# Optimization experiments

Measured on AMD Instinct MI355X. Metric: run time of the kernel, lower is better.

## Reference

```python
import jax, jax.numpy as jnp
import jax.lax as lax
import numpy as np
import math

B, T_FRAMES, H, W = 32, 8, 14, 14
C, CA = 768, 384
L = H * W + 1


def setup_inputs() -> dict:
    key = jax.random.key(0)
    ks = jax.random.split(key, 7)
    s = 0.02
    return {
        "x": jax.random.normal(ks[0], (B * T_FRAMES, L, C), dtype=jnp.float32),
        "W1": jax.random.normal(ks[1], (CA, C), dtype=jnp.float32) * s,
        "b1": jnp.zeros((CA,), dtype=jnp.float32),
        "conv_w": jax.random.normal(ks[2], (CA, 1, 3, 3, 3), dtype=jnp.float32) * s,
        "conv_b": jnp.zeros((CA,), dtype=jnp.float32),
        "W2": jax.random.normal(ks[3], (C, CA), dtype=jnp.float32) * s,
        "b2": jnp.zeros((C,), dtype=jnp.float32),
        "T": T_FRAMES,
    }


def reference(x, W1, b1, conv_w, conv_b, W2, b2, T):
    BT, Lx, Cx = x.shape
    Bb = BT // T
    Ca = W1.shape[0]
    Hh = Ww = int(round(math.sqrt(Lx - 1)))
    # fc1 on all tokens except CLS: [BT, L-1, Ca]
    h = jnp.einsum("blc,ac->bla", x[:, 1:, :], W1) + b1
    # -> [B, Ca, T, H, W] for depthwise 3d conv (groups = Ca)
    h = h.reshape(Bb, T, Hh, Ww, Ca).transpose(0, 4, 1, 2, 3)
    h = lax.conv_general_dilated(
        h, conv_w,
        window_strides=(1, 1, 1),
        padding=[(1, 1), (1, 1), (1, 1)],
        dimension_numbers=("NCDHW", "OIDHW", "NCDHW"),
        feature_group_count=Ca,
    ) + conv_b[None, :, None, None, None]
    # back to [BT, L-1, Ca]
    h = h.transpose(0, 2, 3, 4, 1).reshape(BT, Lx - 1, Ca)
    # fc2: [BT, L-1, C]
    h = jnp.einsum("bla,ca->blc", h, W2) + b2
    # residual add onto non-CLS tokens
    return x.at[:, 1:, :].add(h)
```

## Files before the change

kernel.cpp:

```cpp
#include <hip/hip_runtime.h>
#include <hip/hip_bf16.h>
#include <stdint.h>

#define BTOT   256
#define LX     197
#define CDIM   768
#define CADIM  384
#define TFR    8
#define LM1    196
#define MTOT   50176

typedef unsigned short u16;
typedef short          bf16x8 __attribute__((ext_vector_type(8)));
typedef unsigned short u16x4  __attribute__((ext_vector_type(4)));
typedef unsigned short u16x8  __attribute__((ext_vector_type(8)));
typedef float          f32x4  __attribute__((ext_vector_type(4)));

typedef const __attribute__((address_space(1))) void gvoid_t;
typedef __attribute__((address_space(3))) void       svoid_t;

static __device__ __forceinline__ u16 f2bf(float f) {
  union { float f; uint32_t u; } v; v.f = f;
  uint32_t u = v.u;
  return (u16)((u + 0x7FFFu + ((u >> 16) & 1u)) >> 16);
}
static __device__ __forceinline__ float bf2f(u16 h) {
  union { uint32_t u; float f; } v; v.u = ((uint32_t)h) << 16;
  return v.f;
}
static __device__ __forceinline__ u16 f2bf_hw(float f) {
  union { __hip_bfloat16 b; u16 u; } v;
  v.b = __float2bfloat16(f);
  return v.u;
}

__global__ void prep_small(const float4* __restrict__ x4, float4* __restrict__ out4,
                           const float* __restrict__ W1, const float* __restrict__ W2,
                           const float* __restrict__ cw, u16* __restrict__ w1b,
                           u16* __restrict__ w2b, float* __restrict__ cwT) {
  int i = blockIdx.x * blockDim.x + threadIdx.x;
  if (i < CADIM * CDIM) { w1b[i] = f2bf(W1[i]); w2b[i] = f2bf(W2[i]); }
  if (i < CADIM * 27) {
    int a = i / 27; int tap = i - a * 27;
    cwT[tap * CADIM + a] = cw[i];
  }
  if (i < BTOT * 192) {
    int f = i / 192, v = i - f * 192;
    size_t off = (size_t)f * (LX * CDIM / 4) + v;
    out4[off] = x4[off];
  }
}


__global__ __launch_bounds__(768, 2) void fc1_gemm(
    const float* __restrict__ X,
    const u16* __restrict__ Bw,
    const float* __restrict__ bias,
    u16* __restrict__ Hout)
{
  __shared__ __align__(16) u16 As[2 * 128 * 32];
  __shared__ __align__(16) u16 Bs[2 * 384 * 32];
  const int tid  = threadIdx.x;
  const int lane = tid & 63;
  const int wave = tid >> 6;
  const int m0 = blockIdx.x * 128;
  const int lm = lane & 15;
  const int lk = lane >> 4;
  const int wr = wave / 6;
  const int wc = wave - wr * 6;
  const int wm = wr * 64;
  const int wn = wc * 64;
  const bool is_a = (wave < 4);

  const int g = tid >> 3;
  const int q = tid & 7;
  size_t arow[4];
  int awst[4];
  if (is_a) {
#pragma unroll
    for (int s = 0; s < 4; ++s) {
      int row = g + 32 * s;
      int tok = m0 + row;
      int bt = tok / LM1;
      int l  = tok - bt * LM1;
      arow[s] = (size_t)(bt * LX + 1 + l) * CDIM + q * 4;
      int R    = row >> 1;
      int uu   = (row & 1) * 4 + (q >> 1);
      int slot = uu ^ (R & 7);
      awst[s]  = R * 64 + slot * 8 + (q & 1) * 4;
    }
  }

  const int wb  = wave - 4;
  const int u   = (lane & 7) ^ (lane >> 3);
  const int rr  = 2 * (lane >> 3) + (u >> 2);
  const int cko = (u & 3) * 8;
  size_t boff[3];
  int ldst[3];
  if (!is_a) {
#pragma unroll
    for (int s = 0; s < 3; ++s) {
      int row = wb * 48 + s * 16 + rr;
      boff[s] = (size_t)row * CDIM + cko;
      ldst[s] = (wb * 24 + s * 8) * 64;
    }
  }

  const int lmh   = lm >> 1;
  const int slotp = (((lm & 1) << 2) | lk) ^ lmh;
  const int abase = ((wm >> 1) + lmh) * 64 + slotp * 8;
  const int bbase = ((wn >> 1) + lmh) * 64 + slotp * 8;

  f32x4 acc[4][4];
#pragma unroll
  for (int i = 0; i < 4; i++)
#pragma unroll
    for (int j = 0; j < 4; j++) acc[i][j] = (f32x4)0.0f;

  float4 areg[4];

  if (is_a) {
#pragma unroll
    for (int s = 0; s < 4; ++s) areg[s] = *(const float4*)(X + arow[s]);
#pragma unroll
    for (int s = 0; s < 4; ++s) {
      u16x4 o;
      o[0] = f2bf_hw(areg[s].x); o[1] = f2bf_hw(areg[s].y);
      o[2] = f2bf_hw(areg[s].z); o[3] = f2bf_hw(areg[s].w);
      *(u16x4*)&As[awst[s]] = o;
    }
  } else {
#pragma unroll
    for (int s = 0; s < 3; ++s)
      __builtin_amdgcn_global_load_lds((gvoid_t*)(Bw + boff[s]),
          (svoid_t*)(Bs + ldst[s]), 16, 0, 0);
  }
  __syncthreads();

  int cur = 0;
  for (int kt = 0; kt < 23; ++kt) {
    const int k1 = (kt + 1) * 32;
    const int nb = cur ^ 1;
    if (is_a) {
#pragma unroll
      for (int s = 0; s < 4; ++s) areg[s] = *(const float4*)(X + arow[s] + k1);
    } else {
#pragma unroll
      for (int s = 0; s < 3; ++s)
        __builtin_amdgcn_global_load_lds((gvoid_t*)(Bw + boff[s] + k1),
            (svoid_t*)(Bs + nb * 12288 + ldst[s]), 16, 0, 0);
    }
    {
      const u16* Ab = As + cur * 4096;
      const u16* Bb = Bs + cur * 12288;
      bf16x8 af[4], bfr[4];
#pragma unroll
      for (int i = 0; i < 4; i++) af[i] = *(const bf16x8*)&Ab[abase + i * 512];
#pragma unroll
      for (int j = 0; j < 4; j++) bfr[j] = *(const bf16x8*)&Bb[bbase + j * 512];
#pragma unroll
      for (int i = 0; i < 4; i++)
#pragma unroll
        for (int j = 0; j < 4; j++)
          acc[i][j] = __builtin_amdgcn_mfma_f32_16x16x32_bf16(af[i], bfr[j], acc[i][j], 0, 0, 0);
    }
    if (is_a) {
#pragma unroll
      for (int s = 0; s < 4; ++s) {
        u16x4 o;
        o[0] = f2bf_hw(areg[s].x); o[1] = f2bf_hw(areg[s].y);
        o[2] = f2bf_hw(areg[s].z); o[3] = f2bf_hw(areg[s].w);
        *(u16x4*)&As[nb * 4096 + awst[s]] = o;
      }
    }
    __syncthreads();
    cur ^= 1;
  }
  {
    const u16* Ab = As + cur * 4096;
    const u16* Bb = Bs + cur * 12288;
    bf16x8 af[4], bfr[4];
#pragma unroll
    for (int i = 0; i < 4; i++) af[i] = *(const bf16x8*)&Ab[abase + i * 512];
#pragma unroll
    for (int j = 0; j < 4; j++) bfr[j] = *(const bf16x8*)&Bb[bbase + j * 512];
#pragma unroll
    for (int i = 0; i < 4; i++)
#pragma unroll
      for (int j = 0; j < 4; j++)
        acc[i][j] = __builtin_amdgcn_mfma_f32_16x16x32_bf16(af[i], bfr[j], acc[i][j], 0, 0, 0);
  }

#pragma unroll
  for (int i = 0; i < 4; i++) {
    int rbase = m0 + wm + i * 16 + lk * 4;
#pragma unroll
    for (int j = 0; j < 4; j++) {
      int col = wn + j * 16 + lm;
      float bv = bias[col];
#pragma unroll
      for (int r = 0; r < 4; r++)
        Hout[(rbase + r) * CADIM + col] = f2bf(acc[i][j][r] + bv);
    }
  }
}

__global__ __launch_bounds__(256) void dwconv(
    const u16* __restrict__ h1, const float* __restrict__ cwT,
    const float* __restrict__ cb, u16* __restrict__ h2)
{
  __shared__ __align__(16) u16 lin[3 * 196 * 32];
  const int tid = threadIdx.x;
  const int f   = blockIdx.x;
  const int cc  = blockIdx.y;
  const int tv  = f & 7;

  for (int i = tid; i < 3 * 196 * 4; i += 256) {
    int fd  = i / 784;
    int rem = i - fd * 784;
    int pos = rem >> 2;
    int c8  = rem & 3;
    int tt  = tv + fd - 1;
    u16x8 v = (u16x8)0;
    if (tt >= 0 && tt < TFR) {
      const u16* src = h1 + ((size_t)(f + fd - 1) * LM1 + pos) * CADIM
                          + cc * 32 + c8 * 8;
      v = *(const u16x8*)src;
    }
    *(u16x8*)&lin[(fd * 196 + pos) * 32 + c8 * 8] = v;
  }
  __syncthreads();

  const int cg    = tid & 3;
  const int pidx  = tid >> 2;
  const int cbase = cc * 32 + cg * 8;

  float bv[8];
#pragma unroll
  for (int c = 0; c < 8; ++c) bv[c] = cb[cbase + c];

  float acc[4][8];
  int hk[4], wk[4];
#pragma unroll
  for (int k = 0; k < 4; ++k) {
    int p = pidx + 64 * k;
    hk[k] = p / 14;
    wk[k] = p - hk[k] * 14;
#pragma unroll
    for (int c = 0; c < 8; ++c) acc[k][c] = bv[c];
  }

  for (int dt = 0; dt < 3; ++dt) {
#pragma unroll
    for (int j = 0; j < 9; ++j) {
      const int dh = j / 3 - 1, dw = j % 3 - 1;
      float w8[8];
      const float* wp8 = cwT + (dt * 9 + j) * CADIM + cbase;
#pragma unroll
      for (int c = 0; c < 8; ++c) w8[c] = wp8[c];
#pragma unroll
      for (int k = 0; k < 4; ++k) {
        int p = pidx + 64 * k;
        if (p >= 196) continue;
        int hh = hk[k] + dh, ww = wk[k] + dw;
        if (hh < 0 || hh >= 14 || ww < 0 || ww >= 14) continue;
        const u16x8 v = *(const u16x8*)&lin[(dt * 196 + hh * 14 + ww) * 32 + cg * 8];
#pragma unroll
        for (int c = 0; c < 8; ++c)
          acc[k][c] += bf2f((u16)v[c]) * w8[c];
      }
    }
  }

#pragma unroll
  for (int k = 0; k < 4; ++k) {
    int p = pidx + 64 * k;
    if (p < 196) {
      u16x8 o;
#pragma unroll
      for (int c = 0; c < 8; ++c) o[c] = f2bf(acc[k][c]);
      *(u16x8*)(h2 + ((size_t)f * LM1 + p) * CADIM + cbase) = o;
    }
  }
}

__global__ __launch_bounds__(768, 2) void fc2_gemm(
    const u16* __restrict__ A,
    const u16* __restrict__ Bw,
    const float* __restrict__ bias,
    const float* __restrict__ x,
    float* __restrict__ out)
{
  __shared__ __align__(16) u16 As[2 * 128 * 32];
  __shared__ __align__(16) u16 Bs[2 * 384 * 32];
  const int tid  = threadIdx.x;
  const int lane = tid & 63;
  const int wave = tid >> 6;
  const int m0 = blockIdx.x * 128;
  const int n0 = blockIdx.y * 384;
  const int lm = lane & 15;
  const int lk = lane >> 4;
  const int wr = wave / 6;
  const int wc = wave - wr * 6;
  const int wm = wr * 64;
  const int wn = wc * 64;
  const bool is_a = (wave < 4);

  const int u   = (lane & 7) ^ (lane >> 3);
  const int rr  = 2 * (lane >> 3) + (u >> 2);
  const int cko = (u & 3) * 8;

  size_t aoff[2];
  int lasta[2];
  if (is_a) {
#pragma unroll
    for (int s = 0; s < 2; ++s) {
      int row = wave * 32 + s * 16 + rr;
      aoff[s]  = (size_t)(m0 + row) * CADIM + cko;
      lasta[s] = (wave * 16 + s * 8) * 64;
    }
  }
  const int wb = wave - 4;
  size_t boff[3];
  int ldst[3];
  if (!is_a) {
#pragma unroll
    for (int s = 0; s < 3; ++s) {
      int row = wb * 48 + s * 16 + rr;
      boff[s] = (size_t)(n0 + row) * CADIM + cko;
      ldst[s] = (wb * 24 + s * 8) * 64;
    }
  }

  const int lmh   = lm >> 1;
  const int slotp = (((lm & 1) << 2) | lk) ^ lmh;
  const int abase = ((wm >> 1) + lmh) * 64 + slotp * 8;
  const int bbase = ((wn >> 1) + lmh) * 64 + slotp * 8;

  f32x4 acc[4][4];
#pragma unroll
  for (int i = 0; i < 4; i++)
#pragma unroll
    for (int j = 0; j < 4; j++) acc[i][j] = (f32x4)0.0f;

  if (is_a) {
#pragma unroll
    for (int s = 0; s < 2; ++s)
      __builtin_amdgcn_global_load_lds((gvoid_t*)(A + aoff[s]),
          (svoid_t*)(As + lasta[s]), 16, 0, 0);
  } else {
#pragma unroll
    for (int s = 0; s < 3; ++s)
      __builtin_amdgcn_global_load_lds((gvoid_t*)(Bw + boff[s]),
          (svoid_t*)(Bs + ldst[s]), 16, 0, 0);
  }
  __syncthreads();

  int cur = 0;
  for (int kt = 0; kt < 11; ++kt) {
    const int k1 = (kt + 1) * 32;
    const int nb = cur ^ 1;
    if (is_a) {
#pragma unroll
      for (int s = 0; s < 2; ++s)
        __builtin_amdgcn_global_load_lds((gvoid_t*)(A + aoff[s] + k1),
            (svoid_t*)(As + nb * 4096 + lasta[s]), 16, 0, 0);
    } else {
#pragma unroll
      for (int s = 0; s < 3; ++s)
        __builtin_amdgcn_global_load_lds((gvoid_t*)(Bw + boff[s] + k1),
            (svoid_t*)(Bs + nb * 12288 + ldst[s]), 16, 0, 0);
    }
    {
      const u16* Ab = As + cur * 4096;
      const u16* Bb = Bs + cur * 12288;
      bf16x8 af[4], bfr[4];
#pragma unroll
      for (int i = 0; i < 4; i++) af[i] = *(const bf16x8*)&Ab[abase + i * 512];
#pragma unroll
      for (int j = 0; j < 4; j++) bfr[j] = *(const bf16x8*)&Bb[bbase + j * 512];
#pragma unroll
      for (int i = 0; i < 4; i++)
#pragma unroll
        for (int j = 0; j < 4; j++)
          acc[i][j] = __builtin_amdgcn_mfma_f32_16x16x32_bf16(af[i], bfr[j], acc[i][j], 0, 0, 0);
    }
    __syncthreads();
    cur ^= 1;
  }
  {
    const u16* Ab = As + cur * 4096;
    const u16* Bb = Bs + cur * 12288;
    bf16x8 af[4], bfr[4];
#pragma unroll
    for (int i = 0; i < 4; i++) af[i] = *(const bf16x8*)&Ab[abase + i * 512];
#pragma unroll
    for (int j = 0; j < 4; j++) bfr[j] = *(const bf16x8*)&Bb[bbase + j * 512];
#pragma unroll
    for (int i = 0; i < 4; i++)
#pragma unroll
      for (int j = 0; j < 4; j++)
        acc[i][j] = __builtin_amdgcn_mfma_f32_16x16x32_bf16(af[i], bfr[j], acc[i][j], 0, 0, 0);
  }

  float bve[4];
#pragma unroll
  for (int j = 0; j < 4; j++) bve[j] = bias[n0 + wn + j * 16 + lm];
#pragma unroll
  for (int i = 0; i < 4; i++) {
    int rbase = m0 + wm + i * 16 + lk * 4;
    size_t orow[4];
#pragma unroll
    for (int r = 0; r < 4; r++) {
      int tok = rbase + r;
      int bt = tok / LM1;
      int l  = tok - bt * LM1;
      orow[r] = (size_t)(bt * LX + 1 + l) * CDIM + (n0 + wn + lm);
    }
    float xv[4][4];
#pragma unroll
    for (int r = 0; r < 4; r++)
#pragma unroll
      for (int j = 0; j < 4; j++)
        xv[r][j] = x[orow[r] + j * 16];
#pragma unroll
    for (int r = 0; r < 4; r++)
#pragma unroll
      for (int j = 0; j < 4; j++)
        out[orow[r] + j * 16] = xv[r][j] + acc[i][j][r] + bve[j];
  }
}

extern "C" void kernel_launch(void* const* d_in, const int* in_sizes, int n_in,
                              void* d_out, int out_size, void* d_ws, size_t ws_size,
                              hipStream_t stream) {
  const float* x  = (const float*)d_in[0];
  const float* W1 = (const float*)d_in[1];
  const float* b1 = (const float*)d_in[2];
  const float* cw = (const float*)d_in[3];
  const float* cb = (const float*)d_in[4];
  const float* W2 = (const float*)d_in[5];
  const float* b2 = (const float*)d_in[6];
  float* out = (float*)d_out;

  char* ws = (char*)d_ws;
  u16*   w1b = (u16*)(ws + 0);
  u16*   w2b = (u16*)(ws + 589824);
  float* cwT = (float*)(ws + 1179648);
  u16*   h1  = (u16*)(ws + 1245184);
  u16*   h2  = (u16*)(ws + 39780352);

  prep_small<<<1152, 256, 0, stream>>>((const float4*)x, (float4*)out,
                                       W1, W2, cw, w1b, w2b, cwT);
  fc1_gemm<<<MTOT / 128, 768, 0, stream>>>(x, w1b, b1, h1);
  dwconv  <<<dim3(BTOT, 12), 256, 0, stream>>>(h1, cwT, cb, h2);
  fc2_gemm<<<dim3(MTOT / 128, 2), 768, 0, stream>>>(h2, w2b, b2, x, out);
}
```

Measured before the change: 452.3 us.

## Shrink fc2 GEMM tiles to 128x128 with XCD-aware block swizzle

Result: faster. 434.2 us (-4.0%).

```diff
diff --git a/kernel.cpp b/kernel.cpp
--- a/kernel.cpp
+++ b/kernel.cpp
@@ -284,7 +284,7 @@
   }
 }
 
-__global__ __launch_bounds__(768, 2) void fc2_gemm(
+__global__ __launch_bounds__(256) void fc2_gemm(
     const u16* __restrict__ A,
     const u16* __restrict__ Bw,
     const float* __restrict__ bias,
@@ -292,44 +292,34 @@
     float* __restrict__ out)
 {
   __shared__ __align__(16) u16 As[2 * 128 * 32];
-  __shared__ __align__(16) u16 Bs[2 * 384 * 32];
+  __shared__ __align__(16) u16 Bs[2 * 128 * 32];
   const int tid  = threadIdx.x;
   const int lane = tid & 63;
   const int wave = tid >> 6;
-  const int m0 = blockIdx.x * 128;
-  const int n0 = blockIdx.y * 384;
+
+  const int orig = blockIdx.x;
+  const int lgc  = (orig & 7) * 294 + (orig >> 3);
+  const int lmt  = lgc / 6;
+  const int lnt  = lgc - lmt * 6;
+  const int m0 = lmt * 128;
+  const int n0 = lnt * 128;
+
   const int lm = lane & 15;
   const int lk = lane >> 4;
-  const int wr = wave / 6;
-  const int wc = wave - wr * 6;
-  const int wm = wr * 64;
-  const int wn = wc * 64;
-  const bool is_a = (wave < 4);
+  const int wm = (wave & 1) * 64;
+  const int wn = (wave >> 1) * 64;
 
   const int u   = (lane & 7) ^ (lane >> 3);
   const int rr  = 2 * (lane >> 3) + (u >> 2);
   const int cko = (u & 3) * 8;
-
-  size_t aoff[2];
-  int lasta[2];
-  if (is_a) {
-#pragma unroll
-    for (int s = 0; s < 2; ++s) {
-      int row = wave * 32 + s * 16 + rr;
-      aoff[s]  = (size_t)(m0 + row) * CADIM + cko;
-      lasta[s] = (wave * 16 + s * 8) * 64;
-    }
-  }
-  const int wb = wave - 4;
-  size_t boff[3];
-  int ldst[3];
-  if (!is_a) {
-#pragma unroll
-    for (int s = 0; s < 3; ++s) {
-      int row = wb * 48 + s * 16 + rr;
-      boff[s] = (size_t)(n0 + row) * CADIM + cko;
-      ldst[s] = (wb * 24 + s * 8) * 64;
-    }
+  size_t aoff[2], boff[2];
+  int ldst[2];
+#pragma unroll
+  for (int s = 0; s < 2; ++s) {
+    int row = wave * 32 + s * 16 + rr;
+    aoff[s] = (size_t)(m0 + row) * CADIM + cko;
+    boff[s] = (size_t)(n0 + row) * CADIM + cko;
+    ldst[s] = (wave * 16 + s * 8) * 64;
   }
 
   const int lmh   = lm >> 1;
@@ -343,37 +333,28 @@
 #pragma unroll
     for (int j = 0; j < 4; j++) acc[i][j] = (f32x4)0.0f;
 
-  if (is_a) {
-#pragma unroll
-    for (int s = 0; s < 2; ++s)
-      __builtin_amdgcn_global_load_lds((gvoid_t*)(A + aoff[s]),
-          (svoid_t*)(As + lasta[s]), 16, 0, 0);
-  } else {
-#pragma unroll
-    for (int s = 0; s < 3; ++s)
-      __builtin_amdgcn_global_load_lds((gvoid_t*)(Bw + boff[s]),
-          (svoid_t*)(Bs + ldst[s]), 16, 0, 0);
+#pragma unroll
+  for (int s = 0; s < 2; ++s) {
+    __builtin_amdgcn_global_load_lds((gvoid_t*)(A + aoff[s]),
+        (svoid_t*)(As + ldst[s]), 16, 0, 0);
+    __builtin_amdgcn_global_load_lds((gvoid_t*)(Bw + boff[s]),
+        (svoid_t*)(Bs + ldst[s]), 16, 0, 0);
   }
   __syncthreads();
-
   int cur = 0;
   for (int kt = 0; kt < 11; ++kt) {
     const int k1 = (kt + 1) * 32;
     const int nb = cur ^ 1;
-    if (is_a) {
-#pragma unroll
-      for (int s = 0; s < 2; ++s)
-        __builtin_amdgcn_global_load_lds((gvoid_t*)(A + aoff[s] + k1),
-            (svoid_t*)(As + nb * 4096 + lasta[s]), 16, 0, 0);
-    } else {
-#pragma unroll
-      for (int s = 0; s < 3; ++s)
-        __builtin_amdgcn_global_load_lds((gvoid_t*)(Bw + boff[s] + k1),
-            (svoid_t*)(Bs + nb * 12288 + ldst[s]), 16, 0, 0);
+#pragma unroll
+    for (int s = 0; s < 2; ++s) {
+      __builtin_amdgcn_global_load_lds((gvoid_t*)(A + aoff[s] + k1),
+          (svoid_t*)(As + nb * 4096 + ldst[s]), 16, 0, 0);
+      __builtin_amdgcn_global_load_lds((gvoid_t*)(Bw + boff[s] + k1),
+          (svoid_t*)(Bs + nb * 4096 + ldst[s]), 16, 0, 0);
     }
     {
       const u16* Ab = As + cur * 4096;
-      const u16* Bb = Bs + cur * 12288;
+      const u16* Bb = Bs + cur * 4096;
       bf16x8 af[4], bfr[4];
 #pragma unroll
       for (int i = 0; i < 4; i++) af[i] = *(const bf16x8*)&Ab[abase + i * 512];
@@ -390,7 +371,7 @@
   }
   {
     const u16* Ab = As + cur * 4096;
-    const u16* Bb = Bs + cur * 12288;
+    const u16* Bb = Bs + cur * 4096;
     bf16x8 af[4], bfr[4];
 #pragma unroll
     for (int i = 0; i < 4; i++) af[i] = *(const bf16x8*)&Ab[abase + i * 512];
@@ -403,9 +384,9 @@
         acc[i][j] = __builtin_amdgcn_mfma_f32_16x16x32_bf16(af[i], bfr[j], acc[i][j], 0, 0, 0);
   }
 
-  float bve[4];
-#pragma unroll
-  for (int j = 0; j < 4; j++) bve[j] = bias[n0 + wn + j * 16 + lm];
+  float bv[4];
+#pragma unroll
+  for (int j = 0; j < 4; j++) bv[j] = bias[n0 + wn + j * 16 + lm];
 #pragma unroll
   for (int i = 0; i < 4; i++) {
     int rbase = m0 + wm + i * 16 + lk * 4;
@@ -427,7 +408,7 @@
     for (int r = 0; r < 4; r++)
 #pragma unroll
       for (int j = 0; j < 4; j++)
-        out[orow[r] + j * 16] = xv[r][j] + acc[i][j][r] + bve[j];
+        out[orow[r] + j * 16] = xv[r][j] + acc[i][j][r] + bv[j];
   }
 }
 
@@ -454,5 +435,5 @@
                                        W1, W2, cw, w1b, w2b, cwT);
   fc1_gemm<<<MTOT / 128, 768, 0, stream>>>(x, w1b, b1, h1);
   dwconv  <<<dim3(BTOT, 12), 256, 0, stream>>>(h1, cwT, cb, h2);
-  fc2_gemm<<<dim3(MTOT / 128, 2), 768, 0, stream>>>(h2, w2b, b2, x, out);
-}
+  fc2_gemm<<<2352, 256, 0, stream>>>(h2, w2b, b2, x, out);
+}
```
